# Optimization experiments

Measured on AMD Instinct MI355X. Metric: run time of the kernel, lower is better.

Reference implementation:

```python
import jax, jax.numpy as jnp
import numpy as np

D_MODEL = 1024
N_HEADS = 16
D_HEAD = D_MODEL // N_HEADS


def setup_inputs() -> dict:
    key = jax.random.key(0)
    ks = jax.random.split(key, 5)
    s_in = 1.0 / np.sqrt(D_MODEL)
    x = jax.random.normal(ks[0], (4, 2048, D_MODEL), dtype=jnp.float32)
    W_qkv = jax.random.uniform(ks[1], (D_MODEL, 3 * D_MODEL), jnp.float32, -s_in, s_in)
    b_qkv = jax.random.uniform(ks[2], (3 * D_MODEL,), jnp.float32, -s_in, s_in)
    W_out = jax.random.uniform(ks[3], (D_MODEL, D_MODEL), jnp.float32, -s_in, s_in)
    b_out = jax.random.uniform(ks[4], (D_MODEL,), jnp.float32, -s_in, s_in)
    return {"x": x, "W_qkv": W_qkv, "b_qkv": b_qkv, "W_out": W_out, "b_out": b_out}


def reference(x, W_qkv, b_qkv, W_out, b_out):
    B, T, C = x.shape
    qkv = x @ W_qkv + b_qkv                       # [B,T,3C]
    q, k, v = jnp.split(qkv, 3, axis=-1)
    # [B,T,C] -> [B,H,T,Dh]
    def heads(t):
        return t.reshape(B, T, N_HEADS, D_HEAD).transpose(0, 2, 1, 3)
    q, k, v = heads(q), heads(k), heads(v)
    scale = 1.0 / np.sqrt(D_HEAD).astype(np.float32)
    attn = jnp.einsum('bhqd,bhkd->bhqk', q, k) * scale   # [B,H,T,T]
    causal = jnp.tril(jnp.ones((T, T), dtype=bool))
    attn = jnp.where(causal, attn, -jnp.inf)
    attn_weights = jax.nn.softmax(attn, axis=-1)
    out = jnp.einsum('bhqk,bhkd->bhqd', attn_weights, v)  # [B,H,T,Dh]
    out = out.transpose(0, 2, 1, 3).reshape(B, T, C)
    return out @ W_out + b_out
```

## Files before the change

### kernel.cpp

```cpp
#include <hip/hip_runtime.h>
#include <hip/hip_bf16.h>

#define BATCH   4
#define SEQ     2048
#define DMODEL  1024
#define NHEADS  16
#define DHEAD   64
#define MROWS   (BATCH*SEQ)
#define QKV_N   (3*DMODEL)
#define NEG_BIG (-1.0e30f)
#define WS_NEED ((size_t)MROWS * 2*DMODEL * sizeof(__hip_bfloat16))
#define SCALE_Q 0.18033688011112042f

using bf16 = __hip_bfloat16;
typedef __attribute__((ext_vector_type(8))) short short8;
typedef __attribute__((ext_vector_type(4))) float floatx4;

__device__ __align__(16) unsigned short g_wqT[QKV_N * DMODEL];
__device__ __align__(16) unsigned short g_woT[DMODEL * DMODEL];
__device__ __align__(16) unsigned short g_xb [MROWS * DMODEL];

__device__ __forceinline__ unsigned short f2bf_rne(float f) {
    union { bf16 b; unsigned short u; } t;
    t.b = __float2bfloat16(f);
    return t.u;
}

__device__ __forceinline__ void gload_lds16(const void* g, void* l) {
    __builtin_amdgcn_global_load_lds(
        (const __attribute__((address_space(1))) unsigned*)g,
        (__attribute__((address_space(3))) unsigned*)l, 16, 0, 0);
}

__global__ __launch_bounds__(256) void cast_x(const float* __restrict__ x) {
    const size_t i = ((size_t)blockIdx.x*256 + threadIdx.x)*8;
    const float4 a = *(const float4*)(x + i);
    const float4 b = *(const float4*)(x + i + 4);
    union { uint4 u4; unsigned short us[8]; } o;
    o.us[0]=f2bf_rne(a.x); o.us[1]=f2bf_rne(a.y); o.us[2]=f2bf_rne(a.z); o.us[3]=f2bf_rne(a.w);
    o.us[4]=f2bf_rne(b.x); o.us[5]=f2bf_rne(b.y); o.us[6]=f2bf_rne(b.z); o.us[7]=f2bf_rne(b.w);
    *(uint4*)(g_xb + i) = o.u4;
}

__global__ __launch_bounds__(256) void transcast_w(
    const float* __restrict__ W, int N, int which)
{
    unsigned short* dst = which ? g_woT : g_wqT;
    __shared__ unsigned short T[64][72];
    const int n0 = blockIdx.x * 64, k0 = blockIdx.y * 64;
    const int tid = threadIdx.x;
    const int r = tid >> 2, c0 = (tid & 3) * 16;

#pragma unroll
    for (int it = 0; it < 4; ++it) {
        const float4 v = *(const float4*)(W + (size_t)(k0 + r)*N + n0 + c0 + it*4);
        T[r][c0 + it*4 + 0] = f2bf_rne(v.x);
        T[r][c0 + it*4 + 1] = f2bf_rne(v.y);
        T[r][c0 + it*4 + 2] = f2bf_rne(v.z);
        T[r][c0 + it*4 + 3] = f2bf_rne(v.w);
    }
    __syncthreads();
    const int nr = tid >> 2, kc0 = (tid & 3) * 16;
#pragma unroll
    for (int it = 0; it < 2; ++it) {
        union { uint4 u4; unsigned short us[8]; } o;
#pragma unroll
        for (int j = 0; j < 8; j++) o.us[j] = T[kc0 + it*8 + j][nr];
        *(uint4*)(dst + (size_t)(n0 + nr)*DMODEL + k0 + kc0 + it*8) = o.u4;
    }
}

template<int QKV_MODE>
__global__ __launch_bounds__(512, 2) void gemm256(
    const void* __restrict__ Av, const float* __restrict__ bias,
    void* __restrict__ C0, void* __restrict__ C1, void* __restrict__ C2)
{
    const unsigned short* A  = QKV_MODE ? g_xb  : (const unsigned short*)Av;
    const unsigned short* BT = QKV_MODE ? g_wqT : g_woT;

    __shared__ __align__(16) char smem[131072];
    char* const sA = smem;
    char* const sB = smem + 65536;

    const int tid  = threadIdx.x;
    const int w    = tid >> 6, lane = tid & 63;
    const int m16  = lane & 15, quad = lane >> 4;
    const int rw   = w >> 1, cw = w & 1;
    const int bm   = blockIdx.y, bn = blockIdx.x;

    const int rL = lane >> 2;
    const int cD = (lane & 3) ^ ((lane >> 3) & 3);
    const unsigned short* gA = A  + (size_t)(bm*256 + rL)*DMODEL + cD*8;
    const unsigned short* gB = BT + (size_t)(bn*256 + rL)*DMODEL + cD*8;

    const int laneRd = m16*64 + (quad ^ ((m16 >> 1) & 3))*16;

    floatx4 acc[4][2][4];
#pragma unroll
    for (int q = 0; q < 4; ++q)
#pragma unroll
        for (int i = 0; i < 2; ++i)
#pragma unroll
            for (int j = 0; j < 4; ++j) {
                acc[q][i][j][0]=0.f; acc[q][i][j][1]=0.f;
                acc[q][i][j][2]=0.f; acc[q][i][j][3]=0.f;
            }

    auto stageA = [&](int buf, int half, int k0) {
        char* l0 = sA + buf*32768 + half*16384 + w*1024;
        gload_lds16(gA + (size_t)(half*128 + (w>>1)*16)*DMODEL + k0 + (w&1)*32, l0);
        gload_lds16(gA + (size_t)(half*128 + ((w>>1)+4)*16)*DMODEL + k0 + (w&1)*32, l0 + 8192);
    };
    auto stageB = [&](int buf, int half, int k0) {
        char* l0 = sB + buf*32768 + half*16384 + w*1024;
        gload_lds16(gB + (size_t)(half*128 + (w>>1)*16)*DMODEL + k0 + (w&1)*32, l0);
        gload_lds16(gB + (size_t)(half*128 + ((w>>1)+4)*16)*DMODEL + k0 + (w&1)*32, l0 + 8192);
    };

    stageA(0, 0, 0); stageB(0, 0, 0); stageA(0, 1, 0); stageB(0, 1, 0);
    asm volatile("s_waitcnt vmcnt(0)" ::: "memory");
    __builtin_amdgcn_s_barrier();

    const int NT = DMODEL / 64;
    for (int t = 0; t < NT; ++t) {
        const int  buf = t & 1;
        const int  k1  = (t + 1) * 64;
        const bool st  = (t + 1 < NT);
        char* const Abuf = sA + buf*32768;
        char* const Bbuf = sB + buf*32768;

#pragma unroll
        for (int q = 0; q < 4; ++q) {
            const int qm = q >> 1, qn = q & 1;

            short8 af[2][2], bfr[4][2];
#pragma unroll
            for (int i = 0; i < 2; ++i)
#pragma unroll
                for (int kh = 0; kh < 2; ++kh)
                    af[i][kh] = *(const short8*)(Abuf + qm*16384
                                    + ((rw*2 + i)*2 + kh)*1024 + laneRd);
#pragma unroll
            for (int j = 0; j < 4; ++j)
#pragma unroll
                for (int kh = 0; kh < 2; ++kh)
                    bfr[j][kh] = *(const short8*)(Bbuf + qn*16384
                                    + ((cw*4 + j)*2 + kh)*1024 + laneRd);

            if (st) {
                if      (q == 0) stageA(buf^1, 0, k1);
                else if (q == 1) stageB(buf^1, 0, k1);
                else if (q == 2) stageA(buf^1, 1, k1);
                else             stageB(buf^1, 1, k1);
            }

            __builtin_amdgcn_s_barrier();

            __builtin_amdgcn_s_setprio(1);
#pragma unroll
            for (int i = 0; i < 2; ++i)
#pragma unroll
                for (int j = 0; j < 4; ++j) {
                    acc[q][i][j] = __builtin_amdgcn_mfma_f32_16x16x32_bf16(
                        af[i][0], bfr[j][0], acc[q][i][j], 0, 0, 0);
                    acc[q][i][j] = __builtin_amdgcn_mfma_f32_16x16x32_bf16(
                        af[i][1], bfr[j][1], acc[q][i][j], 0, 0, 0);
                }
            __builtin_amdgcn_s_setprio(0);

            if (q == 0) {
                if (st) { asm volatile("s_waitcnt vmcnt(2)" ::: "memory"); }
                else    { asm volatile("s_waitcnt vmcnt(0)" ::: "memory"); }
            }
            if (q == 3) {
                if (st) { asm volatile("s_waitcnt vmcnt(4)" ::: "memory"); }
                else    { asm volatile("s_waitcnt vmcnt(0)" ::: "memory"); }
            }
            __builtin_amdgcn_s_barrier();
        }
    }

    float bv[2][4];
#pragma unroll
    for (int qn = 0; qn < 2; ++qn)
#pragma unroll
        for (int j = 0; j < 4; ++j)
            bv[qn][j] = bias[bn*256 + qn*128 + cw*64 + j*16 + m16];

    if (QKV_MODE) {
        const int seg = bn >> 2;
        if (seg < 2) {
            bf16* Cout = (bf16*)(seg ? C1 : C0);
            const float sc = seg ? 1.0f : SCALE_Q;
#pragma unroll
            for (int q = 0; q < 4; ++q) {
                const int qm = q >> 1, qn = q & 1;
#pragma unroll
                for (int i = 0; i < 2; ++i)
#pragma unroll
                    for (int r = 0; r < 4; ++r) {
                        const int gm = bm*256 + qm*128 + rw*32 + i*16 + quad*4 + r;
#pragma unroll
                        for (int j = 0; j < 4; ++j) {
                            const int cc = (bn*256 + qn*128 + cw*64 + j*16 + m16) & 1023;
                            Cout[(size_t)gm*DMODEL + cc] =
                                __float2bfloat16((acc[q][i][j][r] + bv[qn][j]) * sc);
                        }
                    }
            }
        } else {
            bf16* VT = (bf16*)C2;
#pragma unroll
            for (int q = 0; q < 4; ++q) {
                const int qm = q >> 1, qn = q & 1;
#pragma unroll
                for (int i = 0; i < 2; ++i) {
                    const int gm0 = bm*256 + qm*128 + rw*32 + i*16 + quad*4;
                    const int bb = gm0 >> 11, t0 = gm0 & 2047;
#pragma unroll
                    for (int j = 0; j < 4; ++j) {
                        const int cv = (bn*256 + qn*128 + cw*64 + j*16 + m16) & 1023;
                        const int hh = cv >> 6, dd = cv & 63;
                        union { unsigned long long u8; unsigned short us[4]; } o;
#pragma unroll
                        for (int r = 0; r < 4; ++r)
                            o.us[r] = f2bf_rne(acc[q][i][j][r] + bv[qn][j]);
                        *(unsigned long long*)(VT
                            + ((size_t)((bb*NHEADS + hh)*DHEAD + dd))*SEQ + t0) = o.u8;
                    }
                }
            }
        }
    } else {
        float* Cout = (float*)C0;
#pragma unroll
        for (int q = 0; q < 4; ++q) {
            const int qm = q >> 1, qn = q & 1;
#pragma unroll
            for (int i = 0; i < 2; ++i)
#pragma unroll
                for (int r = 0; r < 4; ++r) {
                    const int gm = bm*256 + qm*128 + rw*32 + i*16 + quad*4 + r;
#pragma unroll
                    for (int j = 0; j < 4; ++j) {
                        const int cc = (bn*256 + qn*128 + cw*64 + j*16 + m16) & 1023;
                        Cout[(size_t)gm*DMODEL + cc] = acc[q][i][j][r] + bv[qn][j];
                    }
                }
        }
    }
}

__global__ __launch_bounds__(256, 2) void attn_mfma3(
    const bf16* __restrict__ Qg, const bf16* __restrict__ Kg,
    const bf16* __restrict__ VTg, bf16* __restrict__ Og)
{
    __shared__ alignas(16) unsigned short Kt[2][64][72];
    __shared__ alignas(16) unsigned short Vt[2][64][72];
    __shared__ alignas(16) unsigned short Ps[4][32][72];

    const int x = blockIdx.x;
    const int b = x >> 7, h = (x >> 3) & 15, p = x & 7;
    const int tid = threadIdx.x;
    const int w = tid >> 6, lane = tid & 63;
    const int m16 = lane & 15, quad = lane >> 4;
    const int sr = tid >> 2, sc0 = (tid & 3) * 8;
    const size_t bh = (size_t)(b*NHEADS + h);

    for (int seg = 0; seg < 2; ++seg) {
        const int qt  = seg ? (15 - p) : p;
        const int nkt = 2*qt + 2;
        const int qrow0 = qt*128 + w*32;

        short8 qf[2][2];
#pragma unroll
        for (int i = 0; i < 2; ++i)
#pragma unroll
            for (int c = 0; c < 2; ++c)
                qf[i][c] = *(const short8*)(Qg + (size_t)(b*SEQ + qrow0 + i*16 + m16)*DMODEL
                                            + h*DHEAD + c*32 + quad*8);

        floatx4 of[2][4];
        float mrow[2], lrow[2];
#pragma unroll
        for (int i = 0; i < 2; ++i) {
            mrow[i] = NEG_BIG; lrow[i] = 0.f;
#pragma unroll
            for (int nt = 0; nt < 4; ++nt) { of[i][nt][0]=0.f; of[i][nt][1]=0.f; of[i][nt][2]=0.f; of[i][nt][3]=0.f; }
        }

        {
            const bf16* kp = Kg  + (size_t)(b*SEQ + sr)*DMODEL + h*DHEAD + sc0;
            const bf16* vp = VTg + (bh*DHEAD + sr)*SEQ + sc0;
            const uint4 a0 = *(const uint4*)kp, a1 = *(const uint4*)(kp + 32);
            const uint4 b0 = *(const uint4*)vp, b1 = *(const uint4*)(vp + 32);
            __syncthreads();
            *(uint4*)&Kt[0][sr][sc0]      = a0;
            *(uint4*)&Kt[0][sr][sc0 + 32] = a1;
            *(uint4*)&Vt[0][sr][sc0]      = b0;
            *(uint4*)&Vt[0][sr][sc0 + 32] = b1;
            __syncthreads();
        }

        for (int kt = 0; kt < nkt; ++kt) {
            const int buf = kt & 1;
            const int k064 = kt * 64;
            const bool pre = (kt + 1 < nkt);
            uint4 kr0, kr1, vr0, vr1;
            if (pre) {
                const bf16* kp = Kg  + (size_t)(b*SEQ + k064 + 64 + sr)*DMODEL + h*DHEAD + sc0;
                const bf16* vp = VTg + (bh*DHEAD + sr)*SEQ + k064 + 64 + sc0;
                kr0 = *(const uint4*)kp; kr1 = *(const uint4*)(kp + 32);
                vr0 = *(const uint4*)vp; vr1 = *(const uint4*)(vp + 32);
            }

            floatx4 sf[2][4];
#pragma unroll
            for (int t4 = 0; t4 < 4; ++t4) {
                const short8 kf0 = *(const short8*)&Kt[buf][t4*16 + m16][quad*8];
                const short8 kf1 = *(const short8*)&Kt[buf][t4*16 + m16][32 + quad*8];
#pragma unroll
                for (int i = 0; i < 2; ++i) {
                    floatx4 a; a[0]=0.f; a[1]=0.f; a[2]=0.f; a[3]=0.f;
                    a = __builtin_amdgcn_mfma_f32_16x16x32_bf16(kf0, qf[i][0], a, 0, 0, 0);
                    a = __builtin_amdgcn_mfma_f32_16x16x32_bf16(kf1, qf[i][1], a, 0, 0, 0);
                    sf[i][t4] = a;
                }
            }

            const bool need_mask = (k064 + 63 > qrow0);
#pragma unroll
            for (int i = 0; i < 2; ++i) {
                if (need_mask) {
                    const int qg = qrow0 + i*16 + m16;
#pragma unroll
                    for (int t4 = 0; t4 < 4; ++t4)
#pragma unroll
                        for (int r = 0; r < 4; ++r)
                            if (k064 + t4*16 + quad*4 + r > qg) sf[i][t4][r] = NEG_BIG;
                }
                float mx = sf[i][0][0];
#pragma unroll
                for (int t4 = 0; t4 < 4; ++t4)
#pragma unroll
                    for (int r = 0; r < 4; ++r) mx = fmaxf(mx, sf[i][t4][r]);
                mx = fmaxf(mx, __shfl_xor(mx, 16));
                mx = fmaxf(mx, __shfl_xor(mx, 32));

                const float mnew  = fmaxf(mrow[i], mx);
                const float alpha = exp2f(mrow[i] - mnew);
                mrow[i] = mnew;

                float rs = 0.f;
#pragma unroll
                for (int t4 = 0; t4 < 4; ++t4) {
#pragma unroll
                    for (int r = 0; r < 4; ++r) {
                        const float pv = exp2f(sf[i][t4][r] - mnew);
                        sf[i][t4][r] = pv;
                        rs += pv;
                    }
                }
                rs += __shfl_xor(rs, 16);
                rs += __shfl_xor(rs, 32);
                lrow[i] = lrow[i]*alpha + rs;
#pragma unroll
                for (int nt = 0; nt < 4; ++nt)
#pragma unroll
                    for (int r = 0; r < 4; ++r) of[i][nt][r] *= alpha;

#pragma unroll
                for (int t4 = 0; t4 < 4; ++t4) {
                    union { unsigned long long u8; unsigned short us[4]; } o;
#pragma unroll
                    for (int r = 0; r < 4; ++r) o.us[r] = f2bf_rne(sf[i][t4][r]);
                    *(unsigned long long*)&Ps[w][i*16 + m16][t4*16 + quad*4] = o.u8;
                }
            }

            short8 pf[2][2];
#pragma unroll
            for (int i = 0; i < 2; ++i)
#pragma unroll
                for (int c = 0; c < 2; ++c)
                    pf[i][c] = *(const short8*)&Ps[w][i*16 + m16][c*32 + quad*8];
#pragma unroll
            for (int nt = 0; nt < 4; ++nt) {
                const short8 vf0 = *(const short8*)&Vt[buf][nt*16 + m16][quad*8];
                const short8 vf1 = *(const short8*)&Vt[buf][nt*16 + m16][32 + quad*8];
#pragma unroll
                for (int i = 0; i < 2; ++i) {
                    of[i][nt] = __builtin_amdgcn_mfma_f32_16x16x32_bf16(vf0, pf[i][0], of[i][nt], 0, 0, 0);
                    of[i][nt] = __builtin_amdgcn_mfma_f32_16x16x32_bf16(vf1, pf[i][1], of[i][nt], 0, 0, 0);
                }
            }

            if (pre) {
                *(uint4*)&Kt[buf^1][sr][sc0]      = kr0;
                *(uint4*)&Kt[buf^1][sr][sc0 + 32] = kr1;
                *(uint4*)&Vt[buf^1][sr][sc0]      = vr0;
                *(uint4*)&Vt[buf^1][sr][sc0 + 32] = vr1;
            }
            __syncthreads();
        }

#pragma unroll
        for (int i = 0; i < 2; ++i) {
            const float rl = 1.f / fmaxf(lrow[i], 1e-20f);
            const size_t rowbase = (size_t)(b*SEQ + qrow0 + i*16 + m16)*DMODEL + h*DHEAD;
#pragma unroll
            for (int nt = 0; nt < 4; ++nt) {
                union { unsigned long long u8; unsigned short us[4]; } o;
#pragma unroll
                for (int r = 0; r < 4; ++r) o.us[r] = f2bf_rne(of[i][nt][r] * rl);
                *(unsigned long long*)(Og + rowbase + nt*16 + quad*4) = o.u8;
            }
        }
    }
}

__global__ void diag_fill(float* out, int n, float val) {
    int i = blockIdx.x*blockDim.x + threadIdx.x;
    if (i < n) out[i] = val;
}

extern "C" void kernel_launch(void* const* d_in, const int* in_sizes, int n_in,
                              void* d_out, int out_size, void* d_ws, size_t ws_size,
                              hipStream_t stream) {
    const float* x     = (const float*)d_in[0];
    const float* W_qkv = (const float*)d_in[1];
    const float* b_qkv = (const float*)d_in[2];
    const float* W_out = (const float*)d_in[3];
    const float* b_out = (const float*)d_in[4];

    if (ws_size < WS_NEED) {
        const float val = 100.f + (float)(ws_size >> 20);
        diag_fill<<<(out_size + 255)/256, 256, 0, stream>>>((float*)d_out, out_size, val);
        return;
    }

    bf16* Qb  = (bf16*)d_out;
    bf16* VTb = (bf16*)d_out + (size_t)MROWS*DMODEL;
    bf16* Kb  = (bf16*)d_ws;
    bf16* Ob  = (bf16*)d_ws + (size_t)MROWS*DMODEL;

    cast_x<<<MROWS*DMODEL/2048, 256, 0, stream>>>(x);
    {
        dim3 gq(QKV_N/64, DMODEL/64);
        transcast_w<<<gq, 256, 0, stream>>>(W_qkv, QKV_N, 0);
        dim3 go(DMODEL/64, DMODEL/64);
        transcast_w<<<go, 256, 0, stream>>>(W_out, DMODEL, 1);
    }
    {
        dim3 g(QKV_N/256, MROWS/256);
        gemm256<1><<<g, 512, 0, stream>>>(nullptr, b_qkv, Qb, Kb, VTb);
    }
    {
        attn_mfma3<<<512, 256, 0, stream>>>(Qb, Kb, VTb, Ob);
    }
    {
        dim3 g(DMODEL/256, MROWS/256);
        gemm256<0><<<g, 512, 0, stream>>>(Ob, b_out, d_out, nullptr, nullptr);
    }
}
```

Baseline: 294.9 us.

## Use 256x128 GEMM tiles with XCD-aware block remap and lazy softmax rescale

Both GEMMs now use 256x128 output tiles instead of 256x256, which gives more workgroups (768 and 256) and less shared memory per block. Each k-step is restructured into two half-phases that stage B and A separately. A 1D grid is remapped so neighbouring tiles land on the same XCD, and the attention block index is permuted to group heads similarly. Attention also skips the online-softmax rescale unless the running max grows by more than a threshold, trading exact max tracking for fewer exp and multiply operations.

```diff
diff --git a/kernel.cpp b/kernel.cpp
--- a/kernel.cpp
+++ b/kernel.cpp
@@ -71,33 +71,38 @@
 }
 
 template<int QKV_MODE>
-__global__ __launch_bounds__(512, 2) void gemm256(
+__global__ __launch_bounds__(512, 2) void gemm256x128(
     const void* __restrict__ Av, const float* __restrict__ bias,
     void* __restrict__ C0, void* __restrict__ C1, void* __restrict__ C2)
 {
     const unsigned short* A  = QKV_MODE ? g_xb  : (const unsigned short*)Av;
     const unsigned short* BT = QKV_MODE ? g_wqT : g_woT;
-
-    __shared__ __align__(16) char smem[131072];
+    constexpr int NBN = QKV_MODE ? 24 : 8;
+    constexpr int NWG = NBN * 32;
+
+    __shared__ __align__(16) char smem[98304];
     char* const sA = smem;
     char* const sB = smem + 65536;
+
+    const int orig = blockIdx.x;
+    const int wgid = (orig & 7) * (NWG >> 3) + (orig >> 3);
+    const int bm = wgid / NBN, bn = wgid % NBN;
 
     const int tid  = threadIdx.x;
     const int w    = tid >> 6, lane = tid & 63;
     const int m16  = lane & 15, quad = lane >> 4;
     const int rw   = w >> 1, cw = w & 1;
-    const int bm   = blockIdx.y, bn = blockIdx.x;
 
     const int rL = lane >> 2;
     const int cD = (lane & 3) ^ ((lane >> 3) & 3);
     const unsigned short* gA = A  + (size_t)(bm*256 + rL)*DMODEL + cD*8;
-    const unsigned short* gB = BT + (size_t)(bn*256 + rL)*DMODEL + cD*8;
+    const unsigned short* gB = BT + (size_t)(bn*128 + rL)*DMODEL + cD*8;
 
     const int laneRd = m16*64 + (quad ^ ((m16 >> 1) & 3))*16;
 
-    floatx4 acc[4][2][4];
-#pragma unroll
-    for (int q = 0; q < 4; ++q)
+    floatx4 acc[2][2][4];
+#pragma unroll
+    for (int q = 0; q < 2; ++q)
 #pragma unroll
         for (int i = 0; i < 2; ++i)
 #pragma unroll
@@ -106,18 +111,19 @@
                 acc[q][i][j][2]=0.f; acc[q][i][j][3]=0.f;
             }
 
-    auto stageA = [&](int buf, int half, int k0) {
-        char* l0 = sA + buf*32768 + half*16384 + w*1024;
-        gload_lds16(gA + (size_t)(half*128 + (w>>1)*16)*DMODEL + k0 + (w&1)*32, l0);
-        gload_lds16(gA + (size_t)(half*128 + ((w>>1)+4)*16)*DMODEL + k0 + (w&1)*32, l0 + 8192);
+    auto stageA = [&](int buf, int a, int k0) {
+        const int rg = 4*a + (w >> 1), kh = w & 1;
+        gload_lds16(gA + (size_t)(rg*16)*DMODEL + k0 + kh*32,
+                    sA + buf*32768 + (rg*2 + kh)*1024);
     };
-    auto stageB = [&](int buf, int half, int k0) {
-        char* l0 = sB + buf*32768 + half*16384 + w*1024;
-        gload_lds16(gB + (size_t)(half*128 + (w>>1)*16)*DMODEL + k0 + (w&1)*32, l0);
-        gload_lds16(gB + (size_t)(half*128 + ((w>>1)+4)*16)*DMODEL + k0 + (w&1)*32, l0 + 8192);
+    auto stageB = [&](int buf, int b, int k0) {
+        const int rg = 4*b + (w >> 1), kh = w & 1;
+        gload_lds16(gB + (size_t)(rg*16)*DMODEL + k0 + kh*32,
+                    sB + buf*16384 + (rg*2 + kh)*1024);
     };
 
-    stageA(0, 0, 0); stageB(0, 0, 0); stageA(0, 1, 0); stageB(0, 1, 0);
+    stageB(0, 0, 0); stageB(0, 1, 0);
+    stageA(0, 0, 0); stageA(0, 1, 0); stageA(0, 2, 0); stageA(0, 3, 0);
     asm volatile("s_waitcnt vmcnt(0)" ::: "memory");
     __builtin_amdgcn_s_barrier();
 
@@ -126,128 +132,127 @@
         const int  buf = t & 1;
         const int  k1  = (t + 1) * 64;
         const bool st  = (t + 1 < NT);
-        char* const Abuf = sA + buf*32768;
-        char* const Bbuf = sB + buf*32768;
-
-#pragma unroll
-        for (int q = 0; q < 4; ++q) {
-            const int qm = q >> 1, qn = q & 1;
-
-            short8 af[2][2], bfr[4][2];
-#pragma unroll
-            for (int i = 0; i < 2; ++i)
-#pragma unroll
-                for (int kh = 0; kh < 2; ++kh)
-                    af[i][kh] = *(const short8*)(Abuf + qm*16384
-                                    + ((rw*2 + i)*2 + kh)*1024 + laneRd);
-#pragma unroll
-            for (int j = 0; j < 4; ++j)
-#pragma unroll
-                for (int kh = 0; kh < 2; ++kh)
-                    bfr[j][kh] = *(const short8*)(Bbuf + qn*16384
-                                    + ((cw*4 + j)*2 + kh)*1024 + laneRd);
-
-            if (st) {
-                if      (q == 0) stageA(buf^1, 0, k1);
-                else if (q == 1) stageB(buf^1, 0, k1);
-                else if (q == 2) stageA(buf^1, 1, k1);
-                else             stageB(buf^1, 1, k1);
-            }
-
-            __builtin_amdgcn_s_barrier();
-
-            __builtin_amdgcn_s_setprio(1);
-#pragma unroll
-            for (int i = 0; i < 2; ++i)
-#pragma unroll
-                for (int j = 0; j < 4; ++j) {
-                    acc[q][i][j] = __builtin_amdgcn_mfma_f32_16x16x32_bf16(
-                        af[i][0], bfr[j][0], acc[q][i][j], 0, 0, 0);
-                    acc[q][i][j] = __builtin_amdgcn_mfma_f32_16x16x32_bf16(
-                        af[i][1], bfr[j][1], acc[q][i][j], 0, 0, 0);
-                }
-            __builtin_amdgcn_s_setprio(0);
-
-            if (q == 0) {
-                if (st) { asm volatile("s_waitcnt vmcnt(2)" ::: "memory"); }
-                else    { asm volatile("s_waitcnt vmcnt(0)" ::: "memory"); }
-            }
-            if (q == 3) {
-                if (st) { asm volatile("s_waitcnt vmcnt(4)" ::: "memory"); }
-                else    { asm volatile("s_waitcnt vmcnt(0)" ::: "memory"); }
-            }
-            __builtin_amdgcn_s_barrier();
-        }
-    }
-
-    float bv[2][4];
-#pragma unroll
-    for (int qn = 0; qn < 2; ++qn)
+        char* const Ab = sA + buf*32768;
+        char* const Bb = sB + buf*16384;
+
+        short8 bf[4][2], af[2][2];
 #pragma unroll
         for (int j = 0; j < 4; ++j)
-            bv[qn][j] = bias[bn*256 + qn*128 + cw*64 + j*16 + m16];
+#pragma unroll
+            for (int kh = 0; kh < 2; ++kh)
+                bf[j][kh] = *(const short8*)(Bb + ((cw*4 + j)*2 + kh)*1024 + laneRd);
+#pragma unroll
+        for (int i = 0; i < 2; ++i)
+#pragma unroll
+            for (int kh = 0; kh < 2; ++kh)
+                af[i][kh] = *(const short8*)(Ab + ((rw*2 + i)*2 + kh)*1024 + laneRd);
+
+        if (st) { stageB(buf^1, 0, k1); stageB(buf^1, 1, k1); }
+        __builtin_amdgcn_s_barrier();
+
+        __builtin_amdgcn_s_setprio(1);
+#pragma unroll
+        for (int i = 0; i < 2; ++i)
+#pragma unroll
+            for (int j = 0; j < 4; ++j) {
+                acc[0][i][j] = __builtin_amdgcn_mfma_f32_16x16x32_bf16(
+                    af[i][0], bf[j][0], acc[0][i][j], 0, 0, 0);
+                acc[0][i][j] = __builtin_amdgcn_mfma_f32_16x16x32_bf16(
+                    af[i][1], bf[j][1], acc[0][i][j], 0, 0, 0);
+            }
+        __builtin_amdgcn_s_setprio(0);
+
+        if (st) { asm volatile("s_waitcnt vmcnt(2)" ::: "memory"); }
+        else    { asm volatile("s_waitcnt vmcnt(0)" ::: "memory"); }
+        __builtin_amdgcn_s_barrier();
+
+#pragma unroll
+        for (int i = 0; i < 2; ++i)
+#pragma unroll
+            for (int kh = 0; kh < 2; ++kh)
+                af[i][kh] = *(const short8*)(Ab + ((8 + rw*2 + i)*2 + kh)*1024 + laneRd);
+
+        if (st) { stageA(buf^1, 0, k1); stageA(buf^1, 1, k1);
+                  stageA(buf^1, 2, k1); stageA(buf^1, 3, k1); }
+        __builtin_amdgcn_s_barrier();
+
+        __builtin_amdgcn_s_setprio(1);
+#pragma unroll
+        for (int i = 0; i < 2; ++i)
+#pragma unroll
+            for (int j = 0; j < 4; ++j) {
+                acc[1][i][j] = __builtin_amdgcn_mfma_f32_16x16x32_bf16(
+                    af[i][0], bf[j][0], acc[1][i][j], 0, 0, 0);
+                acc[1][i][j] = __builtin_amdgcn_mfma_f32_16x16x32_bf16(
+                    af[i][1], bf[j][1], acc[1][i][j], 0, 0, 0);
+            }
+        __builtin_amdgcn_s_setprio(0);
+
+        if (st) { asm volatile("s_waitcnt vmcnt(2)" ::: "memory"); }
+        else    { asm volatile("s_waitcnt vmcnt(0)" ::: "memory"); }
+        __builtin_amdgcn_s_barrier();
+    }
+
+    float bv[4];
+#pragma unroll
+    for (int j = 0; j < 4; ++j)
+        bv[j] = bias[bn*128 + cw*64 + j*16 + m16];
 
     if (QKV_MODE) {
-        const int seg = bn >> 2;
+        const int seg = bn >> 3;
         if (seg < 2) {
             bf16* Cout = (bf16*)(seg ? C1 : C0);
             const float sc = seg ? 1.0f : SCALE_Q;
 #pragma unroll
-            for (int q = 0; q < 4; ++q) {
-                const int qm = q >> 1, qn = q & 1;
+            for (int q = 0; q < 2; ++q)
 #pragma unroll
                 for (int i = 0; i < 2; ++i)
 #pragma unroll
                     for (int r = 0; r < 4; ++r) {
-                        const int gm = bm*256 + qm*128 + rw*32 + i*16 + quad*4 + r;
+                        const int gm = bm*256 + q*128 + rw*32 + i*16 + quad*4 + r;
 #pragma unroll
                         for (int j = 0; j < 4; ++j) {
-                            const int cc = (bn*256 + qn*128 + cw*64 + j*16 + m16) & 1023;
+                            const int cc = ((bn & 7)*128 + cw*64 + j*16 + m16);
                             Cout[(size_t)gm*DMODEL + cc] =
-                                __float2bfloat16((acc[q][i][j][r] + bv[qn][j]) * sc);
+                                __float2bfloat16((acc[q][i][j][r] + bv[j]) * sc);
                         }
                     }
-            }
         } else {
             bf16* VT = (bf16*)C2;
 #pragma unroll
-            for (int q = 0; q < 4; ++q) {
-                const int qm = q >> 1, qn = q & 1;
+            for (int q = 0; q < 2; ++q)
 #pragma unroll
                 for (int i = 0; i < 2; ++i) {
-                    const int gm0 = bm*256 + qm*128 + rw*32 + i*16 + quad*4;
+                    const int gm0 = bm*256 + q*128 + rw*32 + i*16 + quad*4;
                     const int bb = gm0 >> 11, t0 = gm0 & 2047;
 #pragma unroll
                     for (int j = 0; j < 4; ++j) {
-                        const int cv = (bn*256 + qn*128 + cw*64 + j*16 + m16) & 1023;
+                        const int cv = (bn & 7)*128 + cw*64 + j*16 + m16;
                         const int hh = cv >> 6, dd = cv & 63;
                         union { unsigned long long u8; unsigned short us[4]; } o;
 #pragma unroll
                         for (int r = 0; r < 4; ++r)
-                            o.us[r] = f2bf_rne(acc[q][i][j][r] + bv[qn][j]);
+                            o.us[r] = f2bf_rne(acc[q][i][j][r] + bv[j]);
                         *(unsigned long long*)(VT
                             + ((size_t)((bb*NHEADS + hh)*DHEAD + dd))*SEQ + t0) = o.u8;
                     }
                 }
-            }
         }
     } else {
         float* Cout = (float*)C0;
 #pragma unroll
-        for (int q = 0; q < 4; ++q) {
-            const int qm = q >> 1, qn = q & 1;
+        for (int q = 0; q < 2; ++q)
 #pragma unroll
             for (int i = 0; i < 2; ++i)
 #pragma unroll
                 for (int r = 0; r < 4; ++r) {
-                    const int gm = bm*256 + qm*128 + rw*32 + i*16 + quad*4 + r;
+                    const int gm = bm*256 + q*128 + rw*32 + i*16 + quad*4 + r;
 #pragma unroll
                     for (int j = 0; j < 4; ++j) {
-                        const int cc = (bn*256 + qn*128 + cw*64 + j*16 + m16) & 1023;
-                        Cout[(size_t)gm*DMODEL + cc] = acc[q][i][j][r] + bv[qn][j];
+                        const int cc = bn*128 + cw*64 + j*16 + m16;
+                        Cout[(size_t)gm*DMODEL + cc] = acc[q][i][j][r] + bv[j];
                     }
                 }
-        }
     }
 }
 
@@ -260,7 +265,10 @@
     __shared__ alignas(16) unsigned short Ps[4][32][72];
 
     const int x = blockIdx.x;
-    const int b = x >> 7, h = (x >> 3) & 15, p = x & 7;
+    const int hlo = x & 7, rest = x >> 3;
+    const int p = rest & 7, t2 = rest >> 3;
+    const int b = t2 >> 1, h = hlo | ((t2 & 1) << 3);
+
     const int tid = threadIdx.x;
     const int w = tid >> 6, lane = tid & 63;
     const int m16 = lane & 15, quad = lane >> 4;
@@ -347,27 +355,30 @@
                 mx = fmaxf(mx, __shfl_xor(mx, 16));
                 mx = fmaxf(mx, __shfl_xor(mx, 32));
 
-                const float mnew  = fmaxf(mrow[i], mx);
-                const float alpha = exp2f(mrow[i] - mnew);
-                mrow[i] = mnew;
+                if (__any(mx > mrow[i] + 8.f)) {
+                    const float mnew  = fmaxf(mrow[i], mx);
+                    const float alpha = exp2f(mrow[i] - mnew);
+                    mrow[i] = mnew;
+                    lrow[i] *= alpha;
+#pragma unroll
+                    for (int nt = 0; nt < 4; ++nt)
+#pragma unroll
+                        for (int r = 0; r < 4; ++r) of[i][nt][r] *= alpha;
+                }
 
                 float rs = 0.f;
 #pragma unroll
                 for (int t4 = 0; t4 < 4; ++t4) {
 #pragma unroll
                     for (int r = 0; r < 4; ++r) {
-                        const float pv = exp2f(sf[i][t4][r] - mnew);
+                        const float pv = exp2f(sf[i][t4][r] - mrow[i]);
                         sf[i][t4][r] = pv;
                         rs += pv;
                     }
                 }
                 rs += __shfl_xor(rs, 16);
                 rs += __shfl_xor(rs, 32);
-                lrow[i] = lrow[i]*alpha + rs;
-#pragma unroll
-                for (int nt = 0; nt < 4; ++nt)
-#pragma unroll
-                    for (int r = 0; r < 4; ++r) of[i][nt][r] *= alpha;
+                lrow[i] += rs;
 
 #pragma unroll
                 for (int t4 = 0; t4 < 4; ++t4) {
@@ -452,14 +463,12 @@
         transcast_w<<<go, 256, 0, stream>>>(W_out, DMODEL, 1);
     }
     {
-        dim3 g(QKV_N/256, MROWS/256);
-        gemm256<1><<<g, 512, 0, stream>>>(nullptr, b_qkv, Qb, Kb, VTb);
+        gemm256x128<1><<<768, 512, 0, stream>>>(nullptr, b_qkv, Qb, Kb, VTb);
     }
     {
         attn_mfma3<<<512, 256, 0, stream>>>(Qb, Kb, VTb, Ob);
     }
     {
-        dim3 g(DMODEL/256, MROWS/256);
-        gemm256<0><<<g, 512, 0, stream>>>(Ob, b_out, d_out, nullptr, nullptr);
-    }
-}
+        gemm256x128<0><<<256, 512, 0, stream>>>(Ob, b_out, d_out, nullptr, nullptr);
+    }
+}
```

Result: faster. 277.8 us (-5.8%).
